# Performance work log

Measured on AMD Instinct MI355X. Metric: run time of the kernel, lower is better.

Reference implementation:

```python
import jax, jax.numpy as jnp
import numpy as np

N_NODES = 50000
N_EDGES = 800000
NODE_FEATURES = 128
HIDDEN = 64
N_CLASSES = 6


def gcn_conv(x, src, dst, W, b, n_nodes):
    """PyG GCNConv: out = D^{-1/2}(A+I)D^{-1/2} X W + b (self-loops included)."""
    deg = jax.ops.segment_sum(jnp.ones_like(dst, dtype=x.dtype), dst, num_segments=n_nodes)
    dinv = jnp.where(deg > 0, jax.lax.rsqrt(deg), 0.0)  # [N]
    h = x @ W  # [N, out] - transform before gather (fewer bytes moved)
    norm = dinv[src] * dinv[dst]  # [E+N]
    msg = h[src] * norm[:, None]  # [E+N, out]
    out = jax.ops.segment_sum(msg, dst, num_segments=n_nodes)  # [N, out]
    return out + b


def setup_inputs() -> dict:
    key = jax.random.key(0)
    ks = jax.random.split(key, 8)
    x = jax.random.normal(ks[0], (N_NODES, NODE_FEATURES), dtype=jnp.float32)
    edge_index = jax.random.randint(ks[1], (2, N_EDGES), 0, N_NODES, dtype=jnp.int64)
    W1 = jax.random.normal(ks[2], (NODE_FEATURES, HIDDEN), dtype=jnp.float32) * (1.0 / np.sqrt(NODE_FEATURES))
    b1 = jnp.zeros((HIDDEN,), dtype=jnp.float32)
    W2 = jax.random.normal(ks[3], (HIDDEN, HIDDEN), dtype=jnp.float32) * (1.0 / np.sqrt(HIDDEN))
    b2 = jnp.zeros((HIDDEN,), dtype=jnp.float32)
    Wc = jax.random.normal(ks[4], (HIDDEN * N_NODES, N_CLASSES), dtype=jnp.float32) * (1.0 / np.sqrt(HIDDEN * N_NODES))
    bc = jnp.zeros((N_CLASSES,), dtype=jnp.float32)
    return {"x": x, "edge_index": edge_index, "W1": W1, "b1": b1, "W2": W2, "b2": b2, "Wc": Wc, "bc": bc}


def reference(x, edge_index, W1, b1, W2, b2, Wc, bc):
    n_nodes = x.shape[0]
    loops = jnp.arange(n_nodes, dtype=edge_index.dtype)
    src = jnp.concatenate([edge_index[0], loops])
    dst = jnp.concatenate([edge_index[1], loops])
    h = jax.nn.relu(gcn_conv(x, src, dst, W1, b1, n_nodes))
    h = jax.nn.relu(gcn_conv(h, src, dst, W2, b2, n_nodes))
    logits = h.reshape(1, -1) @ Wc + bc  # [1, n_classes]
    return jax.nn.softmax(logits, axis=1)
```

## Files before the change

### kernel.cpp

```cpp
#include <hip/hip_runtime.h>
#include <math.h>


#define NCH 256
#define RBITS 8
#define NR_MAX 256

__device__ __forceinline__ ushort f32_to_bf16(float f) {
  unsigned u = __float_as_uint(f);
  return (ushort)((u + 0x7fffu + ((u >> 16) & 1u)) >> 16);
}
__device__ __forceinline__ float bf16_to_f32(ushort h) {
  return __uint_as_float(((unsigned)h) << 16);
}


__global__ __launch_bounds__(256) void hist_ranges(
    const int* __restrict__ dst, int* __restrict__ ghist, int NR, int E) {
  __shared__ int h[NR_MAX];
  int tid = threadIdx.x, c = blockIdx.x;
  for (int i = tid; i < NR; i += 256) h[i] = 0;
  __syncthreads();
  int E4 = E >> 2;
  int CH4 = (E4 + NCH - 1) / NCH;
  int i0 = c * CH4, i1 = min(i0 + CH4, E4);
  const int4* d4 = (const int4*)dst;
  for (int i = i0 + tid; i < i1; i += 256) {
    int4 d = d4[i];
    atomicAdd(&h[d.x >> RBITS], 1);
    atomicAdd(&h[d.y >> RBITS], 1);
    atomicAdd(&h[d.z >> RBITS], 1);
    atomicAdd(&h[d.w >> RBITS], 1);
  }
  if (c == NCH - 1) {
    for (int e = (E4 << 2) + tid; e < E; e += 256) atomicAdd(&h[dst[e] >> RBITS], 1);
  }
  __syncthreads();
  for (int i = tid; i < NR; i += 256) ghist[i * NCH + c] = h[i];
}


__global__ __launch_bounds__(256) void scatter_ranges(
    const int* __restrict__ src, const int* __restrict__ dst,
    const int* __restrict__ ghist, int* __restrict__ ebuf, int NR, int E) {
  __shared__ int cur[NR_MAX];
  __shared__ int rowpre[NR_MAX + 1];
  int tid = threadIdx.x, c = blockIdx.x;
  if (tid < NR) {
    const int4* row = (const int4*)(ghist + tid * NCH);
    int s = 0;
    for (int q = 0; q < NCH / 4; ++q) { int4 v = row[q]; s += v.x + v.y + v.z + v.w; }
    rowpre[tid + 1] = s;
  }
  __syncthreads();
  if (tid == 0) {
    rowpre[0] = 0;
    for (int i = 1; i <= NR; ++i) rowpre[i] += rowpre[i - 1];
  }
  __syncthreads();
  if (tid < NR) {
    int s = rowpre[tid];
    const int* row = ghist + tid * NCH;
    const int4* row4 = (const int4*)row;
    int c4 = c >> 2;
    for (int q = 0; q < c4; ++q) { int4 v = row4[q]; s += v.x + v.y + v.z + v.w; }
    for (int cc = c4 << 2; cc < c; ++cc) s += row[cc];
    cur[tid] = s;
  }
  __syncthreads();
  int E4 = E >> 2;
  int CH4 = (E4 + NCH - 1) / NCH;
  int i0 = c * CH4, i1 = min(i0 + CH4, E4);
  const int4* d4 = (const int4*)dst;
  const int4* s4 = (const int4*)src;
  for (int i = i0 + tid; i < i1; i += 256) {
    int4 d = d4[i];
    int4 s = s4[i];
    ebuf[atomicAdd(&cur[d.x >> RBITS], 1)] = s.x | ((d.x & 255) << 16);
    ebuf[atomicAdd(&cur[d.y >> RBITS], 1)] = s.y | ((d.y & 255) << 16);
    ebuf[atomicAdd(&cur[d.z >> RBITS], 1)] = s.z | ((d.z & 255) << 16);
    ebuf[atomicAdd(&cur[d.w >> RBITS], 1)] = s.w | ((d.w & 255) << 16);
  }
  if (c == NCH - 1) {
    for (int e = (E4 << 2) + tid; e < E; e += 256)
      ebuf[atomicAdd(&cur[dst[e] >> RBITS], 1)] = src[e] | ((dst[e] & 255) << 16);
  }
}


__global__ __launch_bounds__(1024) void csr_range(
    const int* __restrict__ ebuf, const int* __restrict__ ghist,
    int* __restrict__ offs, ushort* __restrict__ srt, float* __restrict__ dinv,
    int N, int E, int NR) {
  __shared__ int hist[NR_MAX];
  __shared__ int wtot[16];
  __shared__ int rowpre[NR_MAX + 1];
  int r = blockIdx.x;
  int lo = r << RBITS;
  int len = min(1 << RBITS, N - lo);
  int tid = threadIdx.x, lane = tid & 63, wv = tid >> 6;
  if (tid < NR) {
    const int4* row = (const int4*)(ghist + tid * NCH);
    int s = 0;
    for (int q = 0; q < NCH / 4; ++q) { int4 v = row[q]; s += v.x + v.y + v.z + v.w; }
    rowpre[tid + 1] = s;
  }
  if (tid < len) hist[tid] = 0;
  __syncthreads();
  if (tid == 0) {
    rowpre[0] = 0;
    for (int i = 1; i <= NR; ++i) rowpre[i] += rowpre[i - 1];
  }
  __syncthreads();
  int S = rowpre[r], S1 = rowpre[r + 1];
  for (int i = S + tid; i < S1; i += 1024) atomicAdd(&hist[ebuf[i] >> 16], 1);
  __syncthreads();
  int v = (tid < len) ? hist[tid] : 0;
  if (tid < len) dinv[lo + tid] = rsqrtf((float)(v + 1));
  int x = v;
#pragma unroll
  for (int d = 1; d < 64; d <<= 1) { int y = __shfl_up(x, d, 64); if (lane >= d) x += y; }
  if (lane == 63) wtot[wv] = x;
  __syncthreads();
  if (wv == 0 && lane < 16) {
    int t = wtot[lane], xx = t;
#pragma unroll
    for (int d = 1; d < 16; d <<= 1) { int y = __shfl_up(xx, d, 64); if (lane >= d) xx += y; }
    wtot[lane] = xx - t;
  }
  __syncthreads();
  int excl = x - v + wtot[wv];
  if (tid < len) {
    offs[lo + tid] = S + excl;
    hist[tid] = S + excl;
  }
  if (r == 0 && tid == 0) offs[N] = E;
  __syncthreads();
  for (int i = S + tid; i < S1; i += 1024) {
    int e = ebuf[i];
    srt[atomicAdd(&hist[e >> 16], 1)] = (ushort)(e & 0xFFFF);
  }
}


template <int K, int ROWS>
__global__ __launch_bounds__(256) void gemm_scale(
    const float* __restrict__ X, const float* __restrict__ W,
    const float* __restrict__ dinv, ushort* __restrict__ Gb, int N) {
  __shared__ float smw[K * 64];
  __shared__ float xs[ROWS * K];
  int tid = threadIdx.x, lane = tid & 63, wv = tid >> 6;
  for (int idx = tid; idx < K * 16; idx += 256)
    ((float4*)smw)[idx] = ((const float4*)W)[idx];
  int row0 = blockIdx.x * ROWS;
  int base = row0 * K;
  int cnt4 = (min(ROWS * K, N * K - base)) >> 2;
  const float4* X4 = (const float4*)(X + base);
  for (int idx = tid; idx < cnt4; idx += 256) ((float4*)xs)[idx] = X4[idx];
  __syncthreads();

  constexpr int RW = ROWS / 4;
  float acc[RW];
#pragma unroll
  for (int r = 0; r < RW; ++r) acc[r] = 0.f;
  const float* xr = &xs[(wv * RW) * K];
#pragma unroll 4
  for (int k = 0; k < K; ++k) {
    float wval = smw[k * 64 + lane];
#pragma unroll
    for (int r = 0; r < RW; ++r) acc[r] = fmaf(xr[r * K + k], wval, acc[r]);
  }
#pragma unroll
  for (int r = 0; r < RW; ++r) {
    int row = row0 + wv * RW + r;
    if (row < N) Gb[(size_t)row * 64 + lane] = f32_to_bf16(acc[r] * dinv[row]);
  }
}


template <int MODE>
__global__ __launch_bounds__(256) void aggregate(
    const ushort* __restrict__ Gb, const int* __restrict__ offs,
    const ushort* __restrict__ srt, const float* __restrict__ dinv,
    const float* __restrict__ bias, const float* __restrict__ Wx,
    ushort* __restrict__ Gout, float* __restrict__ part, int N) {
  int lane = threadIdx.x & 63, wv = threadIdx.x >> 6;
  int sub = lane >> 4, fl = lane & 15;
  int node = blockIdx.x * 4 + wv;
  const ushort4* G2 = (const ushort4*)Gb;

  if (MODE == 0 && node >= N) return;

  int e0 = 0, e1 = 0;
  if (node < N) { e0 = offs[node]; e1 = offs[node + 1]; }
  int deg = e1 - e0;

  float4 accA = make_float4(0.f, 0.f, 0.f, 0.f);
  float4 accB = make_float4(0.f, 0.f, 0.f, 0.f);
  if (sub == 0 && node < N) {
    ushort4 q = G2[(size_t)node * 16 + fl];
    accA.x = bf16_to_f32(q.x); accA.y = bf16_to_f32(q.y);
    accA.z = bf16_to_f32(q.z); accA.w = bf16_to_f32(q.w);
  }

  int pre = (deg > 0) ? (int)srt[e0 + min(lane, deg - 1)] : 0;

  int dcap = min(deg, 64);
  int base = 0;
  for (; base + 7 < dcap; base += 8) {
    int sA = __shfl(pre, base + sub, 64);
    int sB = __shfl(pre, base + 4 + sub, 64);
    ushort4 qA = G2[(size_t)sA * 16 + fl];
    ushort4 qB = G2[(size_t)sB * 16 + fl];
    accA.x += bf16_to_f32(qA.x); accA.y += bf16_to_f32(qA.y);
    accA.z += bf16_to_f32(qA.z); accA.w += bf16_to_f32(qA.w);
    accB.x += bf16_to_f32(qB.x); accB.y += bf16_to_f32(qB.y);
    accB.z += bf16_to_f32(qB.z); accB.w += bf16_to_f32(qB.w);
  }
  for (; base + 3 < dcap; base += 4) {
    int s = __shfl(pre, base + sub, 64);
    ushort4 q = G2[(size_t)s * 16 + fl];
    accA.x += bf16_to_f32(q.x); accA.y += bf16_to_f32(q.y);
    accA.z += bf16_to_f32(q.z); accA.w += bf16_to_f32(q.w);
  }
  int e = e0 + base;
  for (; e + 3 < e1; e += 4) {
    int s = srt[e + sub];
    ushort4 q = G2[(size_t)s * 16 + fl];
    accA.x += bf16_to_f32(q.x); accA.y += bf16_to_f32(q.y);
    accA.z += bf16_to_f32(q.z); accA.w += bf16_to_f32(q.w);
  }
  int rem = e1 - e;
  if (sub < rem) {
    int s = srt[e + sub];
    ushort4 q = G2[(size_t)s * 16 + fl];
    accA.x += bf16_to_f32(q.x); accA.y += bf16_to_f32(q.y);
    accA.z += bf16_to_f32(q.z); accA.w += bf16_to_f32(q.w);
  }

  float4 acc;
  acc.x = accA.x + accB.x; acc.y = accA.y + accB.y;
  acc.z = accA.z + accB.z; acc.w = accA.w + accB.w;
#pragma unroll
  for (int m = 16; m < 64; m <<= 1) {
    acc.x += __shfl_xor(acc.x, m, 64);
    acc.y += __shfl_xor(acc.y, m, 64);
    acc.z += __shfl_xor(acc.z, m, 64);
    acc.w += __shfl_xor(acc.w, m, 64);
  }

  if (MODE == 0) {
    if (node < N) {
      float dn = dinv[node];
      float4 bb = ((const float4*)bias)[fl];
      float4 r;
      r.x = fmaxf(fmaf(acc.x, dn, bb.x), 0.f);
      r.y = fmaxf(fmaf(acc.y, dn, bb.y), 0.f);
      r.z = fmaxf(fmaf(acc.z, dn, bb.z), 0.f);
      r.w = fmaxf(fmaf(acc.w, dn, bb.w), 0.f);
      float4 o = make_float4(0.f, 0.f, 0.f, 0.f);
#pragma unroll
      for (int t = 0; t < 4; ++t) {
        int g = 4 * sub + t;
        int srcl = (lane & 48) | g;
        float h0 = __shfl(r.x, srcl, 64);
        float h1 = __shfl(r.y, srcl, 64);
        float h2 = __shfl(r.z, srcl, 64);
        float h3 = __shfl(r.w, srcl, 64);
        const float* wp = Wx + (size_t)(4 * g) * 64 + 4 * fl;
        float4 w0 = *(const float4*)(wp);
        float4 w1 = *(const float4*)(wp + 64);
        float4 w2 = *(const float4*)(wp + 128);
        float4 w3 = *(const float4*)(wp + 192);
        o.x = fmaf(h0, w0.x, fmaf(h1, w1.x, fmaf(h2, w2.x, fmaf(h3, w3.x, o.x))));
        o.y = fmaf(h0, w0.y, fmaf(h1, w1.y, fmaf(h2, w2.y, fmaf(h3, w3.y, o.y))));
        o.z = fmaf(h0, w0.z, fmaf(h1, w1.z, fmaf(h2, w2.z, fmaf(h3, w3.z, o.z))));
        o.w = fmaf(h0, w0.w, fmaf(h1, w1.w, fmaf(h2, w2.w, fmaf(h3, w3.w, o.w))));
      }
#pragma unroll
      for (int m = 16; m < 64; m <<= 1) {
        o.x += __shfl_xor(o.x, m, 64);
        o.y += __shfl_xor(o.y, m, 64);
        o.z += __shfl_xor(o.z, m, 64);
        o.w += __shfl_xor(o.w, m, 64);
      }
      if (sub == 0) {
        ushort4 q;
        q.x = f32_to_bf16(o.x * dn);
        q.y = f32_to_bf16(o.y * dn);
        q.z = f32_to_bf16(o.z * dn);
        q.w = f32_to_bf16(o.w * dn);
        ((ushort4*)Gout)[(size_t)node * 16 + fl] = q;
      }
    }
  } else {
    float a[6] = {0.f, 0.f, 0.f, 0.f, 0.f, 0.f};
    if (sub == 0 && node < N) {
      float dn = dinv[node];
      float4 bb = ((const float4*)bias)[fl];
      float4 r;
      r.x = fmaxf(fmaf(acc.x, dn, bb.x), 0.f);
      r.y = fmaxf(fmaf(acc.y, dn, bb.y), 0.f);
      r.z = fmaxf(fmaf(acc.z, dn, bb.z), 0.f);
      r.w = fmaxf(fmaf(acc.w, dn, bb.w), 0.f);
      const float4* w4 = (const float4*)(Wx + (size_t)node * 384 + fl * 24);
      float4 w0 = w4[0], w1 = w4[1], w2 = w4[2], w3 = w4[3], w4_ = w4[4], w5 = w4[5];
      a[0] = fmaf(r.x, w0.x, fmaf(r.y, w1.z, fmaf(r.z, w3.x, r.w * w4_.z)));
      a[1] = fmaf(r.x, w0.y, fmaf(r.y, w1.w, fmaf(r.z, w3.y, r.w * w4_.w)));
      a[2] = fmaf(r.x, w0.z, fmaf(r.y, w2.x, fmaf(r.z, w3.z, r.w * w5.x)));
      a[3] = fmaf(r.x, w0.w, fmaf(r.y, w2.y, fmaf(r.z, w3.w, r.w * w5.y)));
      a[4] = fmaf(r.x, w1.x, fmaf(r.y, w2.z, fmaf(r.z, w4_.x, r.w * w5.z)));
      a[5] = fmaf(r.x, w1.y, fmaf(r.y, w2.w, fmaf(r.z, w4_.y, r.w * w5.w)));
    }
#pragma unroll
    for (int c = 0; c < 6; ++c) {
      for (int d = 32; d > 0; d >>= 1) a[c] += __shfl_down(a[c], d, 64);
    }
    __shared__ float sh[4][6];
    if (lane == 0) {
#pragma unroll
      for (int c = 0; c < 6; ++c) sh[wv][c] = a[c];
    }
    __syncthreads();
    if (threadIdx.x == 0) {
#pragma unroll
      for (int c = 0; c < 6; ++c)
        part[(size_t)blockIdx.x * 6 + c] = sh[0][c] + sh[1][c] + sh[2][c] + sh[3][c];
    }
  }
}

__global__ __launch_bounds__(1024) void reduce_softmax(
    const float* __restrict__ part, int nb,
    const float* __restrict__ bc, float* __restrict__ out) {
  int tid = threadIdx.x, lane = tid & 63, wv = tid >> 6;
  float a[6] = {0.f, 0.f, 0.f, 0.f, 0.f, 0.f};
  for (int b = tid; b < nb; b += 1024) {
    const float* p = part + (size_t)b * 6;
#pragma unroll
    for (int c = 0; c < 6; ++c) a[c] += p[c];
  }
#pragma unroll
  for (int c = 0; c < 6; ++c) {
    for (int d = 32; d > 0; d >>= 1) a[c] += __shfl_down(a[c], d, 64);
  }
  __shared__ float sh[16][6];
  if (lane == 0) {
#pragma unroll
    for (int c = 0; c < 6; ++c) sh[wv][c] = a[c];
  }
  __syncthreads();
  if (tid == 0) {
    float l[6], m = -1e30f;
#pragma unroll
    for (int c = 0; c < 6; ++c) {
      float t = 0.f;
      for (int w = 0; w < 16; ++w) t += sh[w][c];
      l[c] = t + bc[c];
      m = fmaxf(m, l[c]);
    }
    float s = 0.f;
#pragma unroll
    for (int c = 0; c < 6; ++c) { l[c] = __expf(l[c] - m); s += l[c]; }
    float inv = 1.f / s;
#pragma unroll
    for (int c = 0; c < 6; ++c) out[c] = l[c] * inv;
  }
}


static inline size_t align4up(size_t x) { return (x + 3) & ~(size_t)3; }

extern "C" void kernel_launch(void* const* d_in, const int* in_sizes, int n_in,
                              void* d_out, int out_size, void* d_ws, size_t ws_size,
                              hipStream_t stream) {
  const float* x  = (const float*)d_in[0];
  const int*   ei = (const int*)d_in[1];
  const float* W1 = (const float*)d_in[2];
  const float* b1 = (const float*)d_in[3];
  const float* W2 = (const float*)d_in[4];
  const float* b2 = (const float*)d_in[5];
  const float* Wc = (const float*)d_in[6];
  const float* bc = (const float*)d_in[7];
  float* out = (float*)d_out;

  const int N = in_sizes[0] / 128;
  const int E = in_sizes[1] / 2;
  const int* esrc = ei;
  const int* edst = ei + E;
  const int NR = (N + (1 << RBITS) - 1) >> RBITS;
  const int AGRID = (N + 3) / 4;

  size_t o = 0;
  int* offs    = (int*)d_ws + o;            o = align4up(o + N + 1);
  ushort* srt  = (ushort*)((int*)d_ws + o); o = align4up(o + (E + 1) / 2);
  float* dinv  = (float*)d_ws + o;          o = align4up(o + N);
  int* ghist   = (int*)d_ws + o;            o = align4up(o + (size_t)NR * NCH);
  ushort* Gb1  = (ushort*)((int*)d_ws + o); o = align4up(o + (size_t)N * 32);
  ushort* Gb2  = (ushort*)((int*)d_ws + o); o = align4up(o + max((size_t)N * 32, (size_t)E));
  float* part  = (float*)d_ws + o;          o = align4up(o + (size_t)AGRID * 6);
  int* ebuf    = (int*)Gb2;

  hist_ranges<<<NCH, 256, 0, stream>>>(edst, ghist, NR, E);
  scatter_ranges<<<NCH, 256, 0, stream>>>(esrc, edst, ghist, ebuf, NR, E);
  csr_range<<<NR, 1024, 0, stream>>>(ebuf, ghist, offs, srt, dinv, N, E, NR);

  gemm_scale<128, 32><<<(N + 31) / 32, 256, 0, stream>>>(x, W1, dinv, Gb1, N);
  aggregate<0><<<AGRID, 256, 0, stream>>>(Gb1, offs, srt, dinv, b1, W2, Gb2, nullptr, N);
  aggregate<1><<<AGRID, 256, 0, stream>>>(Gb2, offs, srt, dinv, b2, Wc, nullptr, part, N);

  reduce_softmax<<<1, 1024, 0, stream>>>(part, AGRID, bc, out);
}
```

Before: 157.7 us.

## Make aggregate kernels persistent grid-stride with prefetch of next node's edges

The aggregate kernels now launch a fixed grid of 2048 blocks. Each wave walks nodes in a grid-stride loop and prefetches the next node's CSR offsets and neighbor indices while the current node is gathered. In the classifier mode, per-node partial logits are kept in registers across nodes, so the cross-lane reduction and partial write happen once per block rather than once per node. This is meant to hide index-load latency and cut block launch and reduction overhead, at the cost of fewer waves in flight and longer serial per-wave work. The code assumes the first node of every wave is below N, which holds only while N >= 8192.

```diff
diff --git a/kernel.cpp b/kernel.cpp
--- a/kernel.cpp
+++ b/kernel.cpp
@@ -183,76 +183,93 @@
     const ushort* __restrict__ Gb, const int* __restrict__ offs,
     const ushort* __restrict__ srt, const float* __restrict__ dinv,
     const float* __restrict__ bias, const float* __restrict__ Wx,
-    ushort* __restrict__ Gout, float* __restrict__ part, int N) {
+    ushort* __restrict__ Gout, float* __restrict__ part, int N, int NW) {
   int lane = threadIdx.x & 63, wv = threadIdx.x >> 6;
   int sub = lane >> 4, fl = lane & 15;
+  const ushort4* G2 = (const ushort4*)Gb;
+
+  float cls[6] = {0.f, 0.f, 0.f, 0.f, 0.f, 0.f};
+  float4 bb = ((const float4*)bias)[fl];
+
   int node = blockIdx.x * 4 + wv;
-  const ushort4* G2 = (const ushort4*)Gb;
-
-  if (MODE == 0 && node >= N) return;
-
-  int e0 = 0, e1 = 0;
-  if (node < N) { e0 = offs[node]; e1 = offs[node + 1]; }
-  int deg = e1 - e0;
-
-  float4 accA = make_float4(0.f, 0.f, 0.f, 0.f);
-  float4 accB = make_float4(0.f, 0.f, 0.f, 0.f);
-  if (sub == 0 && node < N) {
-    ushort4 q = G2[(size_t)node * 16 + fl];
-    accA.x = bf16_to_f32(q.x); accA.y = bf16_to_f32(q.y);
-    accA.z = bf16_to_f32(q.z); accA.w = bf16_to_f32(q.w);
-  }
-
-  int pre = (deg > 0) ? (int)srt[e0 + min(lane, deg - 1)] : 0;
-
-  int dcap = min(deg, 64);
-  int base = 0;
-  for (; base + 7 < dcap; base += 8) {
-    int sA = __shfl(pre, base + sub, 64);
-    int sB = __shfl(pre, base + 4 + sub, 64);
-    ushort4 qA = G2[(size_t)sA * 16 + fl];
-    ushort4 qB = G2[(size_t)sB * 16 + fl];
-    accA.x += bf16_to_f32(qA.x); accA.y += bf16_to_f32(qA.y);
-    accA.z += bf16_to_f32(qA.z); accA.w += bf16_to_f32(qA.w);
-    accB.x += bf16_to_f32(qB.x); accB.y += bf16_to_f32(qB.y);
-    accB.z += bf16_to_f32(qB.z); accB.w += bf16_to_f32(qB.w);
-  }
-  for (; base + 3 < dcap; base += 4) {
-    int s = __shfl(pre, base + sub, 64);
-    ushort4 q = G2[(size_t)s * 16 + fl];
-    accA.x += bf16_to_f32(q.x); accA.y += bf16_to_f32(q.y);
-    accA.z += bf16_to_f32(q.z); accA.w += bf16_to_f32(q.w);
-  }
-  int e = e0 + base;
-  for (; e + 3 < e1; e += 4) {
-    int s = srt[e + sub];
-    ushort4 q = G2[(size_t)s * 16 + fl];
-    accA.x += bf16_to_f32(q.x); accA.y += bf16_to_f32(q.y);
-    accA.z += bf16_to_f32(q.z); accA.w += bf16_to_f32(q.w);
-  }
-  int rem = e1 - e;
-  if (sub < rem) {
-    int s = srt[e + sub];
-    ushort4 q = G2[(size_t)s * 16 + fl];
-    accA.x += bf16_to_f32(q.x); accA.y += bf16_to_f32(q.y);
-    accA.z += bf16_to_f32(q.z); accA.w += bf16_to_f32(q.w);
-  }
-
-  float4 acc;
-  acc.x = accA.x + accB.x; acc.y = accA.y + accB.y;
-  acc.z = accA.z + accB.z; acc.w = accA.w + accB.w;
-#pragma unroll
-  for (int m = 16; m < 64; m <<= 1) {
-    acc.x += __shfl_xor(acc.x, m, 64);
-    acc.y += __shfl_xor(acc.y, m, 64);
-    acc.z += __shfl_xor(acc.z, m, 64);
-    acc.w += __shfl_xor(acc.w, m, 64);
-  }
-
-  if (MODE == 0) {
-    if (node < N) {
-      float dn = dinv[node];
-      float4 bb = ((const float4*)bias)[fl];
+  int e0 = offs[node], e1 = offs[node + 1];
+  {
+    int dg = e1 - e0;
+    e0 = e0; e1 = e1;
+  }
+  int pre;
+  {
+    int dg = e1 - e0;
+    pre = (dg > 0) ? (int)srt[e0 + min(lane, dg - 1)] : 0;
+  }
+
+  while (true) {
+    int nnode = node + NW;
+    bool nvalid = nnode < N;
+    int ne0 = 0, ne1 = 0;
+    if (nvalid) { ne0 = offs[nnode]; ne1 = offs[nnode + 1]; }
+
+    int deg = e1 - e0;
+    float4 accA = make_float4(0.f, 0.f, 0.f, 0.f);
+    float4 accB = make_float4(0.f, 0.f, 0.f, 0.f);
+    if (sub == 0) {
+      ushort4 q = G2[(size_t)node * 16 + fl];
+      accA.x = bf16_to_f32(q.x); accA.y = bf16_to_f32(q.y);
+      accA.z = bf16_to_f32(q.z); accA.w = bf16_to_f32(q.w);
+    }
+
+    int dcap = min(deg, 64);
+    int base = 0;
+    for (; base + 7 < dcap; base += 8) {
+      int sA = __shfl(pre, base + sub, 64);
+      int sB = __shfl(pre, base + 4 + sub, 64);
+      ushort4 qA = G2[(size_t)sA * 16 + fl];
+      ushort4 qB = G2[(size_t)sB * 16 + fl];
+      accA.x += bf16_to_f32(qA.x); accA.y += bf16_to_f32(qA.y);
+      accA.z += bf16_to_f32(qA.z); accA.w += bf16_to_f32(qA.w);
+      accB.x += bf16_to_f32(qB.x); accB.y += bf16_to_f32(qB.y);
+      accB.z += bf16_to_f32(qB.z); accB.w += bf16_to_f32(qB.w);
+    }
+    for (; base + 3 < dcap; base += 4) {
+      int s = __shfl(pre, base + sub, 64);
+      ushort4 q = G2[(size_t)s * 16 + fl];
+      accA.x += bf16_to_f32(q.x); accA.y += bf16_to_f32(q.y);
+      accA.z += bf16_to_f32(q.z); accA.w += bf16_to_f32(q.w);
+    }
+    int e = e0 + base;
+    for (; e + 3 < e1; e += 4) {
+      int s = srt[e + sub];
+      ushort4 q = G2[(size_t)s * 16 + fl];
+      accA.x += bf16_to_f32(q.x); accA.y += bf16_to_f32(q.y);
+      accA.z += bf16_to_f32(q.z); accA.w += bf16_to_f32(q.w);
+    }
+    int rem = e1 - e;
+    if (sub < rem) {
+      int s = srt[e + sub];
+      ushort4 q = G2[(size_t)s * 16 + fl];
+      accA.x += bf16_to_f32(q.x); accA.y += bf16_to_f32(q.y);
+      accA.z += bf16_to_f32(q.z); accA.w += bf16_to_f32(q.w);
+    }
+
+    int npre = 0;
+    if (nvalid) {
+      int nd = ne1 - ne0;
+      npre = (nd > 0) ? (int)srt[ne0 + min(lane, nd - 1)] : 0;
+    }
+
+    float4 acc;
+    acc.x = accA.x + accB.x; acc.y = accA.y + accB.y;
+    acc.z = accA.z + accB.z; acc.w = accA.w + accB.w;
+#pragma unroll
+    for (int m = 16; m < 64; m <<= 1) {
+      acc.x += __shfl_xor(acc.x, m, 64);
+      acc.y += __shfl_xor(acc.y, m, 64);
+      acc.z += __shfl_xor(acc.z, m, 64);
+      acc.w += __shfl_xor(acc.w, m, 64);
+    }
+
+    float dn = dinv[node];
+    if (MODE == 0) {
       float4 r;
       r.x = fmaxf(fmaf(acc.x, dn, bb.x), 0.f);
       r.y = fmaxf(fmaf(acc.y, dn, bb.y), 0.f);
@@ -292,34 +309,37 @@
         q.w = f32_to_bf16(o.w * dn);
         ((ushort4*)Gout)[(size_t)node * 16 + fl] = q;
       }
-    }
-  } else {
-    float a[6] = {0.f, 0.f, 0.f, 0.f, 0.f, 0.f};
-    if (sub == 0 && node < N) {
-      float dn = dinv[node];
-      float4 bb = ((const float4*)bias)[fl];
-      float4 r;
-      r.x = fmaxf(fmaf(acc.x, dn, bb.x), 0.f);
-      r.y = fmaxf(fmaf(acc.y, dn, bb.y), 0.f);
-      r.z = fmaxf(fmaf(acc.z, dn, bb.z), 0.f);
-      r.w = fmaxf(fmaf(acc.w, dn, bb.w), 0.f);
-      const float4* w4 = (const float4*)(Wx + (size_t)node * 384 + fl * 24);
-      float4 w0 = w4[0], w1 = w4[1], w2 = w4[2], w3 = w4[3], w4_ = w4[4], w5 = w4[5];
-      a[0] = fmaf(r.x, w0.x, fmaf(r.y, w1.z, fmaf(r.z, w3.x, r.w * w4_.z)));
-      a[1] = fmaf(r.x, w0.y, fmaf(r.y, w1.w, fmaf(r.z, w3.y, r.w * w4_.w)));
-      a[2] = fmaf(r.x, w0.z, fmaf(r.y, w2.x, fmaf(r.z, w3.z, r.w * w5.x)));
-      a[3] = fmaf(r.x, w0.w, fmaf(r.y, w2.y, fmaf(r.z, w3.w, r.w * w5.y)));
-      a[4] = fmaf(r.x, w1.x, fmaf(r.y, w2.z, fmaf(r.z, w4_.x, r.w * w5.z)));
-      a[5] = fmaf(r.x, w1.y, fmaf(r.y, w2.w, fmaf(r.z, w4_.y, r.w * w5.w)));
-    }
+    } else {
+      if (sub == 0) {
+        float4 r;
+        r.x = fmaxf(fmaf(acc.x, dn, bb.x), 0.f);
+        r.y = fmaxf(fmaf(acc.y, dn, bb.y), 0.f);
+        r.z = fmaxf(fmaf(acc.z, dn, bb.z), 0.f);
+        r.w = fmaxf(fmaf(acc.w, dn, bb.w), 0.f);
+        const float4* w4 = (const float4*)(Wx + (size_t)node * 384 + fl * 24);
+        float4 w0 = w4[0], w1 = w4[1], w2 = w4[2], w3 = w4[3], w4_ = w4[4], w5 = w4[5];
+        cls[0] = fmaf(r.x, w0.x, fmaf(r.y, w1.z, fmaf(r.z, w3.x, fmaf(r.w, w4_.z, cls[0]))));
+        cls[1] = fmaf(r.x, w0.y, fmaf(r.y, w1.w, fmaf(r.z, w3.y, fmaf(r.w, w4_.w, cls[1]))));
+        cls[2] = fmaf(r.x, w0.z, fmaf(r.y, w2.x, fmaf(r.z, w3.z, fmaf(r.w, w5.x, cls[2]))));
+        cls[3] = fmaf(r.x, w0.w, fmaf(r.y, w2.y, fmaf(r.z, w3.w, fmaf(r.w, w5.y, cls[3]))));
+        cls[4] = fmaf(r.x, w1.x, fmaf(r.y, w2.z, fmaf(r.z, w4_.x, fmaf(r.w, w5.z, cls[4]))));
+        cls[5] = fmaf(r.x, w1.y, fmaf(r.y, w2.w, fmaf(r.z, w4_.y, fmaf(r.w, w5.w, cls[5]))));
+      }
+    }
+
+    if (!nvalid) break;
+    node = nnode; e0 = ne0; e1 = ne1; pre = npre;
+  }
+
+  if (MODE == 1) {
 #pragma unroll
     for (int c = 0; c < 6; ++c) {
-      for (int d = 32; d > 0; d >>= 1) a[c] += __shfl_down(a[c], d, 64);
+      for (int d = 32; d > 0; d >>= 1) cls[c] += __shfl_down(cls[c], d, 64);
     }
     __shared__ float sh[4][6];
     if (lane == 0) {
 #pragma unroll
-      for (int c = 0; c < 6; ++c) sh[wv][c] = a[c];
+      for (int c = 0; c < 6; ++c) sh[wv][c] = cls[c];
     }
     __syncthreads();
     if (threadIdx.x == 0) {
@@ -389,7 +409,8 @@
   const int* esrc = ei;
   const int* edst = ei + E;
   const int NR = (N + (1 << RBITS) - 1) >> RBITS;
-  const int AGRID = (N + 3) / 4;
+  const int AGRID = 2048;
+  const int NW = AGRID * 4;
 
   size_t o = 0;
   int* offs    = (int*)d_ws + o;            o = align4up(o + N + 1);
@@ -406,8 +427,8 @@
   csr_range<<<NR, 1024, 0, stream>>>(ebuf, ghist, offs, srt, dinv, N, E, NR);
 
   gemm_scale<128, 32><<<(N + 31) / 32, 256, 0, stream>>>(x, W1, dinv, Gb1, N);
-  aggregate<0><<<AGRID, 256, 0, stream>>>(Gb1, offs, srt, dinv, b1, W2, Gb2, nullptr, N);
-  aggregate<1><<<AGRID, 256, 0, stream>>>(Gb2, offs, srt, dinv, b2, Wc, nullptr, part, N);
+  aggregate<0><<<AGRID, 256, 0, stream>>>(Gb1, offs, srt, dinv, b1, W2, Gb2, nullptr, N, NW);
+  aggregate<1><<<AGRID, 256, 0, stream>>>(Gb2, offs, srt, dinv, b2, Wc, nullptr, part, N, NW);
 
   reduce_softmax<<<1, 1024, 0, stream>>>(part, AGRID, bc, out);
 }
```

New measurement: 150.8 us. -4.4%, faster.
